# Kernel tuning notes

Hardware: AMD Instinct MI355X
Metric: run time of the kernel (lower is better)

Reference implementation:

```python
import jax, jax.numpy as jnp
import numpy as np
from jax import lax

RHO = 0.1          # init kwarg rho
CG_ITERS = 15      # dc_torch(..., 0.001, 15): fixed 15 CG iterations
EPS = 1e-12


def _c(x):  # (..., 2) real pair -> complex
    return lax.complex(x[..., 0], x[..., 1])


def _r(x):  # complex -> (..., 2) real pair
    return jnp.stack([jnp.real(x), jnp.imag(x)], axis=-1)


def fft2c(x):
    ax = (-2, -1)
    return jnp.fft.fftshift(jnp.fft.fft2(jnp.fft.ifftshift(x, axes=ax), axes=ax, norm='ortho'), axes=ax)


def ifft2c(x):
    ax = (-2, -1)
    return jnp.fft.fftshift(jnp.fft.ifft2(jnp.fft.ifftshift(x, axes=ax), axes=ax, norm='ortho'), axes=ax)


def setup_inputs() -> dict:
    key = jax.random.key(0)
    k0, k1, k2, k3 = jax.random.split(key, 4)
    B, S, C, H, W = 1, 4, 16, 320, 320
    K = jax.random.normal(k0, (B, S, C, H, W, 2), jnp.float32)
    I = jax.random.normal(k1, (B, S, H, W, 2), jnp.float32)
    csm = jax.random.normal(k2, (B, C, H, W, 2), jnp.float32) * 0.2
    mask = (jax.random.uniform(k3, (B, S, H, W)) < 0.35).astype(jnp.float32)
    return {'K_mulShot_sigCoil': K, 'I': I, 'csm': csm, 'mask': mask}


def _dc_cg(kdata, img, s, m):
    # kdata: [B,S,C,H,W] complex, img: [B,S,H,W], s: [B,C,H,W], m: [B,S,H,W]
    def E(x):                      # image [B,S,H,W] -> k-space [B,S,C,H,W]
        return m[:, :, None] * fft2c(s[:, None] * x[:, :, None])

    def EH(y):                     # adjoint: coil-combine
        return jnp.sum(jnp.conj(s)[:, None] * ifft2c(m[:, :, None] * y), axis=2)

    def AtA(x):
        return EH(E(x)) + RHO * x

    rhs = EH(kdata) + RHO * img
    x0 = jnp.zeros_like(rhs)
    r0 = rhs
    rs0 = jnp.real(jnp.vdot(r0, r0))

    def body(carry, _):
        x, r, p, rs = carry
        Ap = AtA(p)
        alpha = rs / (jnp.real(jnp.vdot(p, Ap)) + EPS)
        x = x + alpha * p
        r = r - alpha * Ap
        rs_new = jnp.real(jnp.vdot(r, r))
        p = r + (rs_new / (rs + EPS)) * p
        return (x, r, p, rs_new), None

    (x, _, _, _), _ = lax.scan(body, (x0, r0, r0, rs0), None, length=CG_ITERS)
    return x


def reference(K_mulShot_sigCoil, I, csm, mask):
    kdata = _c(K_mulShot_sigCoil)
    img = _c(I)
    s = _c(csm)
    x = _dc_cg(kdata, img, s, mask)   # image-domain CG solution
    K = fft2c(x)                      # sf.dc_torch returns k-space
    out = ifft2c(K)                   # layer returns I = ifft2c(K)
    return _r(out)
```

## Files before the change

### kernel.cpp

```cpp
#include <hip/hip_runtime.h>
#include <math.h>


#define NDIM 320
#define HHALF 160
#define HW (NDIM*NDIM)
#define NS 4
#define NC 16
#define RHO_ 0.1f
#define CG_ITERS 15

typedef float v2f __attribute__((ext_vector_type(2)));
typedef _Float16 h2 __attribute__((ext_vector_type(2)));
typedef _Float16 h8v __attribute__((ext_vector_type(8)));

__device__ __forceinline__ v2f h2f(h2 h){ return (v2f){(float)h.x, (float)h.y}; }
__device__ __forceinline__ h2 f2h(v2f v){ return (h2){(_Float16)v.x, (_Float16)v.y}; }

__device__ __forceinline__ void wsync(){
    __builtin_amdgcn_fence(__ATOMIC_ACQ_REL, "wavefront");
    __builtin_amdgcn_wave_barrier();
}

__device__ __forceinline__ float wred(float v){
    #pragma unroll
    for (int o=32;o>0;o>>=1) v += __shfl_down(v,o,64);
    return v;
}

__device__ __forceinline__ v2f cmulf(v2f a, v2f b){
    return (v2f){a.x,a.x}*b + (v2f){-a.y,a.y}*(v2f){b.y,b.x};
}

template<int SIGMA>
__device__ __forceinline__ v2f cmulw(v2f a, v2f w){
    v2f wb = (SIGMA<0) ? w : (v2f){w.x, -w.y};
    return cmulf(a, wb);
}

template<int SIGMA>
__device__ __forceinline__ v2f mulj(v2f z){
    return (v2f){ -(float)SIGMA*z.y, (float)SIGMA*z.x };
}

template<int SIGMA>
__device__ __forceinline__ void radix5(const v2f* u, v2f* v){
    const float C1 = 0.30901699437494742f, S1 = 0.95105651629515357f;
    const float C2 = -0.80901699437494745f, S2 = 0.58778525229247312f;
    v2f t1=u[1]+u[4], t2=u[2]+u[3], t3=u[1]-u[4], t4=u[2]-u[3];
    v[0] = u[0] + t1 + t2;
    v2f m1 = u[0] + t1*C1 + t2*C2;
    v2f m2 = u[0] + t1*C2 + t2*C1;
    v2f n1 = t3*S1 + t4*S2;
    v2f n2 = t3*S2 - t4*S1;
    v2f j1 = mulj<SIGMA>(n1), j2 = mulj<SIGMA>(n2);
    v[1]=m1+j1; v[4]=m1-j1; v[2]=m2+j2; v[3]=m2-j2;
}

template<int SIGMA>
__device__ __forceinline__ void dft8(const v2f* u, v2f* y){
    const float C = 0.70710678118654752f;
    v2f a0=u[0]+u[4], a1=u[0]-u[4];
    v2f a2=u[2]+u[6], a3=u[2]-u[6];
    v2f a4=u[1]+u[5], a5=u[1]-u[5];
    v2f a6=u[3]+u[7], a7=u[3]-u[7];
    v2f j3 = mulj<SIGMA>(a3);
    v2f E0=a0+a2, E2=a0-a2;
    v2f E1=a1+j3, E3=a1-j3;
    v2f j7 = mulj<SIGMA>(a7);
    v2f O0=a4+a6, O2=a4-a6;
    v2f O1=a5+j7, O3=a5-j7;
    v2f W1 = (O1 + mulj<SIGMA>(O1)) * C;
    v2f jO2 = mulj<SIGMA>(O2);
    v2f W3 = (mulj<SIGMA>(O3) - O3) * C;
    y[0]=E0+O0; y[4]=E0-O0;
    y[1]=E1+W1; y[5]=E1-W1;
    y[2]=E2+jO2; y[6]=E2-jO2;
    y[3]=E3+W3; y[7]=E3-W3;
}

template<int SIGMA>
__device__ __forceinline__ void s1_from_regs(v2f* __restrict__ A, int t,
                                             const v2f* u5){
    v2f v[5];
    radix5<SIGMA>(u5, v);
    #pragma unroll
    for (int c=0;c<5;++c) A[5*t + c] = v[c];
}

template<int SIGMA>
__device__ __forceinline__ void s1_stage(v2f* __restrict__ A, int t){
    v2f u[5];
    #pragma unroll
    for (int q=0;q<5;++q) u[q] = A[t + 64*q];
    wsync();
    s1_from_regs<SIGMA>(A, t, u);
}

template<int SIGMA>
__device__ __forceinline__ void s2_stage(v2f* __restrict__ A, int t, v2f w40){
    if (t < 40){
        v2f u[8];
        #pragma unroll
        for (int q=0;q<8;++q) u[q] = A[t + 40*q];
        wsync();
        v2f wc = w40;
        u[1] = cmulw<SIGMA>(u[1], wc);
        #pragma unroll
        for (int q=2;q<8;++q){ wc = cmulf(wc, w40); u[q] = cmulw<SIGMA>(u[q], wc); }
        v2f v[8];
        dft8<SIGMA>(u, v);
        int k = t % 5, jb = t / 5;
        int base = jb*40 + k;
        #pragma unroll
        for (int c=0;c<8;++c) A[base + 5*c] = v[c];
    }
}

template<int SIGMA>
__device__ __forceinline__ void s3_toregs(const v2f* __restrict__ A, int t,
                                          v2f w320, v2f* v){
    if (t < 40){
        v2f u[8];
        #pragma unroll
        for (int q=0;q<8;++q) u[q] = A[t + 40*q];
        v2f wc = w320;
        u[1] = cmulw<SIGMA>(u[1], wc);
        #pragma unroll
        for (int q=2;q<8;++q){ wc = cmulf(wc, w320); u[q] = cmulw<SIGMA>(u[q], wc); }
        dft8<SIGMA>(u, v);
    }
}

template<int SIGMA>
__device__ __forceinline__ void a3_fromregs(v2f* __restrict__ A, int t,
                                            v2f w320, const v2f* vin){
    if (t < 40){
        v2f u[8];
        dft8<SIGMA>(vin, u);
        v2f wc = w320;
        u[1] = cmulw<SIGMA>(u[1], wc);
        #pragma unroll
        for (int q=2;q<8;++q){ wc = cmulf(wc, w320); u[q] = cmulw<SIGMA>(u[q], wc); }
        #pragma unroll
        for (int q=0;q<8;++q) A[t + 40*q] = u[q];
    }
}

template<int SIGMA>
__device__ __forceinline__ void a2_stage(v2f* __restrict__ A, int t, v2f w40){
    if (t < 40){
        int k = t % 5, jb = t / 5;
        int base = jb*40 + k;
        v2f v[8];
        #pragma unroll
        for (int c=0;c<8;++c) v[c] = A[base + 5*c];
        wsync();
        v2f u[8];
        dft8<SIGMA>(v, u);
        v2f wc = w40;
        u[1] = cmulw<SIGMA>(u[1], wc);
        #pragma unroll
        for (int q=2;q<8;++q){ wc = cmulf(wc, w40); u[q] = cmulw<SIGMA>(u[q], wc); }
        #pragma unroll
        for (int q=0;q<8;++q) A[t + 40*q] = u[q];
    }
}

template<int SIGMA>
__device__ __forceinline__ void a1_toregs(const v2f* __restrict__ A, int t,
                                          v2f* out5){
    v2f v[5];
    #pragma unroll
    for (int c=0;c<5;++c) v[c] = A[5*t + c];
    radix5<SIGMA>(v, out5);
}

__device__ __forceinline__ void make_w(int t, v2f& w40, v2f& w320){
    float sn, cs;
    const float n2pi = -6.283185307179586f;
    __sincosf(n2pi*(float)(t%5)/40.f, &sn, &cs); w40  = (v2f){cs, sn};
    __sincosf(n2pi*(float)t/320.f,    &sn, &cs); w320 = (v2f){cs, sn};
}

__device__ __forceinline__ int sh160(int i){ return i < HHALF ? i + HHALF : i - HHALF; }

__global__ void k_prep(const v2f* __restrict__ kin, const float* __restrict__ mask,
                       const v2f* __restrict__ csm, h2* __restrict__ sP,
                       float* __restrict__ mscT, h2* __restrict__ K,
                       float* __restrict__ scal)
{
    int gid = blockIdx.x*blockDim.x + threadIdx.x;
    int gsz = gridDim.x*blockDim.x;
    if (gid < 64) scal[gid] = 0.f;
    for (int i = gid; i < NC*HW; i += gsz){
        int w = i % NDIM; int h = (i/NDIM) % NDIM; int c = i/HW;
        sP[i] = f2h(csm[(c*NDIM + sh160(h))*NDIM + sh160(w)]);
    }
    for (int i = gid; i < NS*HW; i += gsz){
        int h = i % NDIM; int wc = (i/NDIM)%NDIM; int s = i/HW;
        float m = mask[(s*NDIM + sh160(h))*NDIM + sh160(wc)];
        mscT[i] = m*m*(1.0f/102400.0f);
    }
    for (int i = gid; i < NS*NC*HW; i += gsz){
        int w = i % NDIM; int h = (i/NDIM)%NDIM; int sc = i/HW;
        int s = sc >> 4;
        int hs = sh160(h), ws = sh160(w);
        float m = mask[(s*NDIM + hs)*NDIM + ws];
        v2f kv = kin[((long)sc*NDIM + hs)*NDIM + ws];
        float f = m*(1.0f/320.0f);
        K[i] = f2h(kv * f);
    }
}

__global__ __launch_bounds__(256) void k_passA(
    const v2f* __restrict__ rv_, const v2f* __restrict__ pOld,
    v2f* __restrict__ pNew, const h2* __restrict__ sP,
    h2* __restrict__ K, float* __restrict__ scal, int iter)
{
    int bid = blockIdx.x;
    int cg = bid & 3;
    int hg = (bid>>2) % 80;
    int s  = bid / (4*80);
    int tid = threadIdx.x; int rl = tid>>6; int t = tid&63;
    int h = hg*4 + rl;
    __shared__ v2f bufA[4][NDIM];
    v2f* A = &bufA[rl][0];
    v2f w40, w320; make_w(t, w40, w320);
    float beta = 0.f;
    if (iter > 0) beta = scal[iter] / (scal[iter-1] + 1e-12f);
    long base = (long)s*HW + h*NDIM;
    v2f pv[5];
    #pragma unroll
    for (int j=0;j<5;++j){
        int idx = t + 64*j;
        v2f rr = rv_[base+idx];
        if (iter > 0){
            v2f pp = pOld[base+idx];
            pv[j] = rr + pp*beta;
        } else pv[j] = rr;
    }
    if (cg == 0){
        float d = 0.f;
        #pragma unroll
        for (int j=0;j<5;++j){
            pNew[base + t + 64*j] = pv[j];
            d += pv[j].x*pv[j].x + pv[j].y*pv[j].y;
        }
        float wd = wred(d);
        if (t==0) atomicAdd(&scal[16+iter], RHO_*wd);
    }
    int c = cg*4;
    const h2* srow = sP + (long)c*HW + h*NDIM;
    v2f sv[5];
    #pragma unroll
    for (int j=0;j<5;++j) sv[j] = h2f(srow[t+64*j]);
    #pragma unroll
    for (int c0=0;c0<4;++c0){
        v2f u5[5];
        #pragma unroll
        for (int j=0;j<5;++j) u5[j] = cmulf(sv[j], pv[j]);
        v2f sv2[5];
        if (c0<3){
            const h2* sr2 = srow + (long)(c0+1)*HW;
            #pragma unroll
            for (int j=0;j<5;++j) sv2[j] = h2f(sr2[t+64*j]);
        }
        wsync();
        s1_from_regs<-1>(A, t, u5);
        wsync();
        s2_stage<-1>(A, t, w40);
        wsync();
        v2f v8[8];
        s3_toregs<-1>(A, t, w320, v8);
        long kb = ((long)(s*NC + c + c0))*HW + h*NDIM;
        if (t < 40){
            #pragma unroll
            for (int cc=0;cc<8;++cc) K[kb + t + 40*cc] = f2h(v8[cc]);
        }
        if (c0<3){
            #pragma unroll
            for (int j=0;j<5;++j) sv[j]=sv2[j];
        }
    }
}

__global__ __launch_bounds__(1024) void k_passB(h2* __restrict__ K,
    const float* __restrict__ mscT, int doMask)
{
    constexpr int L = 324;
    int bid = blockIdx.x;
    int wt = bid % 20;
    int sc = bid / 20;
    int s = sc >> 4;
    int tid = threadIdx.x;
    int col = tid >> 6;
    int t = tid & 63;
    int w0 = wt*16;
    __shared__ v2f bufA[16][L];
    v2f w40, w320; make_w(t, w40, w320);
    float mv[8];
    if (doMask && t < 40){
        const float* mcol = mscT + (long)s*HW + (long)(w0+col)*NDIM;
        #pragma unroll
        for (int cc=0;cc<8;++cc) mv[cc] = mcol[t+40*cc];
    }
    long gb = (long)sc*HW + w0;
    for (int i = tid; i < NDIM*4; i += 1024){
        int row = i >> 2, ch = i & 3;
        h8v val = *(const h8v*)&K[gb + (long)row*NDIM + ch*4];
        #pragma unroll
        for (int k=0;k<4;++k)
            bufA[ch*4+k][row] = (v2f){(float)val[2*k], (float)val[2*k+1]};
    }
    __syncthreads();
    v2f* A = &bufA[col][0];
    if (doMask){
        s1_stage<-1>(A, t);
        wsync();
        s2_stage<-1>(A, t, w40);
        wsync();
        v2f v8[8];
        s3_toregs<-1>(A, t, w320, v8);
        if (t < 40){
            #pragma unroll
            for (int cc=0;cc<8;++cc) v8[cc] = v8[cc]*mv[cc];
        }
        wsync();
        a3_fromregs<1>(A, t, w320, v8);
        wsync();
        a2_stage<1>(A, t, w40);
        wsync();
        v2f x5[5];
        a1_toregs<1>(A, t, x5);
        wsync();
        #pragma unroll
        for (int q=0;q<5;++q) A[t + 64*q] = x5[q];
    } else {
        s1_stage<1>(A, t);
        wsync();
        s2_stage<1>(A, t, w40);
        wsync();
        v2f v8[8];
        s3_toregs<1>(A, t, w320, v8);
        wsync();
        if (t < 40){
            #pragma unroll
            for (int cc=0;cc<8;++cc) A[t + 40*cc] = v8[cc];
        }
    }
    __syncthreads();
    for (int i = tid; i < NDIM*4; i += 1024){
        int row = i >> 2, ch = i & 3;
        h8v val;
        #pragma unroll
        for (int k=0;k<4;++k){
            v2f u = bufA[ch*4+k][row];
            val[2*k] = (_Float16)u.x; val[2*k+1] = (_Float16)u.y;
        }
        *(h8v*)&K[gb + (long)row*NDIM + ch*4] = val;
    }
}

__global__ __launch_bounds__(256) void k_passC2(
    const h2* __restrict__ K, const h2* __restrict__ sP,
    const v2f* __restrict__ pVec, v2f* __restrict__ part,
    float* __restrict__ scal, int dotSlot, int doDot)
{
    int bid = blockIdx.x;
    int cg = bid & 3;
    int hg = (bid>>2) % 80;
    int s  = bid / (4*80);
    int tid = threadIdx.x; int rl = tid>>6; int t = tid&63;
    int h = hg*4 + rl;
    __shared__ v2f bufA[4][NDIM];
    __shared__ float redS[4];
    v2f* A = &bufA[rl][0];
    v2f w40, w320; make_w(t, w40, w320);
    int c = cg*4;
    long kb0 = ((long)(s*NC + c))*HW + h*NDIM;
    const h2* srow = sP + (long)c*HW + h*NDIM;
    v2f kv[8], sv[5];
    if (t < 40){
        #pragma unroll
        for (int cc=0;cc<8;++cc) kv[cc] = h2f(K[kb0 + t + 40*cc]);
    }
    #pragma unroll
    for (int j=0;j<5;++j) sv[j] = h2f(srow[t+64*j]);
    v2f acc[5];
    #pragma unroll
    for (int j=0;j<5;++j) acc[j]=(v2f){0.f,0.f};
    #pragma unroll
    for (int c0=0;c0<4;++c0){
        a3_fromregs<1>(A, t, w320, kv);
        v2f kv2[8], sv2[5];
        if (c0<3){
            long kb = kb0 + (long)(c0+1)*HW;
            const h2* sr2 = srow + (long)(c0+1)*HW;
            if (t < 40){
                #pragma unroll
                for (int cc=0;cc<8;++cc) kv2[cc] = h2f(K[kb + t + 40*cc]);
            }
            #pragma unroll
            for (int j=0;j<5;++j) sv2[j] = h2f(sr2[t+64*j]);
        }
        wsync();
        a2_stage<1>(A, t, w40);
        wsync();
        v2f x5[5];
        a1_toregs<1>(A, t, x5);
        #pragma unroll
        for (int j=0;j<5;++j){
            acc[j] += (v2f){sv[j].x,sv[j].x}*x5[j]
                    + (v2f){sv[j].y,-sv[j].y}*(v2f){x5[j].y,x5[j].x};
        }
        wsync();
        if (c0<3){
            #pragma unroll
            for (int cc=0;cc<8;++cc) kv[cc]=kv2[cc];
            #pragma unroll
            for (int j=0;j<5;++j) sv[j]=sv2[j];
        }
    }
    long pbase = (long)s*HW + h*NDIM;
    long obase = ((long)cg*NS + s)*HW + h*NDIM;
    float dot = 0.f;
    #pragma unroll
    for (int j=0;j<5;++j){
        int idx=t+64*j;
        part[obase+idx] = acc[j];
        if (doDot){
            v2f pp = pVec[pbase+idx];
            dot += pp.x*acc[j].x + pp.y*acc[j].y;
        }
    }
    if (doDot){
        float wd = wred(dot);
        if (t==0) redS[rl] = wd;
        __syncthreads();
        if (tid==0) atomicAdd(&scal[dotSlot], redS[0]+redS[1]+redS[2]+redS[3]);
    }
}

__global__ __launch_bounds__(256) void k_rhs_fin(
    const v2f* __restrict__ part, const v2f* __restrict__ Iin,
    v2f* __restrict__ r, v2f* __restrict__ x, float* __restrict__ scal)
{
    __shared__ float red[256];
    int gid = blockIdx.x*blockDim.x + threadIdx.x;
    int gsz = gridDim.x*blockDim.x;
    float rs = 0.f;
    const int NV = NS*HW;
    for (int i = gid; i < NV; i += gsz){
        int w = i % NDIM; int h = (i/NDIM)%NDIM; int s = i/HW;
        v2f iv = Iin[((long)s*NDIM + sh160(h))*NDIM + sh160(w)];
        v2f rr = part[i] + part[NV+i] + part[2*NV+i] + part[3*NV+i] + iv*RHO_;
        r[i] = rr;
        x[i] = (v2f){0.f,0.f};
        rs += rr.x*rr.x + rr.y*rr.y;
    }
    red[threadIdx.x]=rs; __syncthreads();
    for (int o=128;o>0;o>>=1){ if (threadIdx.x<o) red[threadIdx.x]+=red[threadIdx.x+o]; __syncthreads(); }
    if (threadIdx.x==0) atomicAdd(&scal[0], red[0]);
}

__global__ __launch_bounds__(256) void k_update(
    v2f* __restrict__ x, v2f* __restrict__ r,
    const v2f* __restrict__ p, const v2f* __restrict__ part,
    float* __restrict__ scal, int iter)
{
    __shared__ float red[256];
    float alpha = scal[iter] / (scal[16+iter] + 1e-12f);
    int gid = blockIdx.x*blockDim.x + threadIdx.x;
    int gsz = gridDim.x*blockDim.x;
    float rs = 0.f;
    const int NV = NS*HW;
    for (int i = gid; i < NV; i += gsz){
        v2f pvv=p[i];
        v2f av = part[i] + part[NV+i] + part[2*NV+i] + part[3*NV+i] + pvv*RHO_;
        v2f xv = x[i] + pvv*alpha;
        v2f rv = r[i] - av*alpha;
        x[i]=xv; r[i]=rv;
        rs += rv.x*rv.x + rv.y*rv.y;
    }
    red[threadIdx.x]=rs; __syncthreads();
    for (int o=128;o>0;o>>=1){ if (threadIdx.x<o) red[threadIdx.x]+=red[threadIdx.x+o]; __syncthreads(); }
    if (threadIdx.x==0) atomicAdd(&scal[iter+1], red[0]);
}

__global__ void k_final(const v2f* __restrict__ x, v2f* __restrict__ out)
{
    int gid = blockIdx.x*blockDim.x + threadIdx.x;
    int gsz = gridDim.x*blockDim.x;
    for (int i = gid; i < NS*HW; i += gsz){
        int w = i % NDIM; int h = (i/NDIM)%NDIM; int s = i/HW;
        out[i] = x[(long)s*HW + sh160(h)*NDIM + sh160(w)];
    }
}

extern "C" void kernel_launch(void* const* d_in, const int* in_sizes, int n_in,
                              void* d_out, int out_size, void* d_ws, size_t ws_size,
                              hipStream_t stream) {
    (void)in_sizes; (void)n_in; (void)out_size; (void)ws_size;
    const v2f* kin  = (const v2f*)d_in[0];
    const v2f* Iin  = (const v2f*)d_in[1];
    const v2f* csm  = (const v2f*)d_in[2];
    const float* mask = (const float*)d_in[3];

    char* w = (char*)d_ws;
    size_t off = 0;
    float* scal = (float*)(w+off);  off += 1024;
    h2* sP    = (h2*)(w+off);  off += (size_t)NC*HW*4;
    float* mscT = (float*)(w+off); off += (size_t)NS*HW*4;
    h2* K     = (h2*)(w+off);  off += (size_t)NS*NC*HW*4;
    v2f* x    = (v2f*)(w+off); off += (size_t)NS*HW*8;
    v2f* r    = (v2f*)(w+off); off += (size_t)NS*HW*8;
    v2f* pA   = (v2f*)(w+off); off += (size_t)NS*HW*8;
    v2f* pB   = (v2f*)(w+off); off += (size_t)NS*HW*8;
    v2f* part = (v2f*)(w+off); off += (size_t)4*NS*HW*8;

    k_prep<<<2048,256,0,stream>>>(kin, mask, csm, sP, mscT, K, scal);
    k_passB<<<NS*NC*20,1024,0,stream>>>(K, mscT, 0);
    k_passC2<<<NS*80*4,256,0,stream>>>(K, sP, r, part, scal, 63, 0);
    k_rhs_fin<<<640,256,0,stream>>>(part, Iin, r, x, scal);

    for (int it=0; it<CG_ITERS; ++it){
        v2f* pNew = (it&1)? pB : pA;
        v2f* pOld = (it&1)? pA : pB;
        k_passA<<<NS*80*4,256,0,stream>>>(r, pOld, pNew, sP, K, scal, it);
        k_passB<<<NS*NC*20,1024,0,stream>>>(K, mscT, 1);
        k_passC2<<<NS*80*4,256,0,stream>>>(K, sP, pNew, part, scal, 16+it, 1);
        k_update<<<640,256,0,stream>>>(x, r, pNew, part, scal, it);
    }
    k_final<<<512,256,0,stream>>>(x, (v2f*)d_out);
}
```

Measured before the change: 1.538 ms.

## Pad FFT LDS rows against bank conflicts and process two columns per wave

All shared-memory FFT buffers now use a padded row stride and a skewed index (one extra slot every 16 elements) to cut LDS bank conflicts in the strided radix-5/radix-8 stage accesses. In the column-FFT kernel each wavefront now handles two columns, with reads and writes of the two columns interleaved, and the block shrinks from 1024 to 512 threads with a higher occupancy hint. This is meant to raise instruction-level parallelism and LDS throughput. The cost is more registers per thread, plus one extra wave barrier per stage from splitting each stage into separate read and write phases.

```diff
diff --git a/kernel.cpp b/kernel.cpp
--- a/kernel.cpp
+++ b/kernel.cpp
@@ -9,6 +9,7 @@
 #define NC 16
 #define RHO_ 0.1f
 #define CG_ITERS 15
+#define LPAD 341
 
 typedef float v2f __attribute__((ext_vector_type(2)));
 typedef _Float16 h2 __attribute__((ext_vector_type(2)));
@@ -16,6 +17,8 @@
 
 __device__ __forceinline__ v2f h2f(h2 h){ return (v2f){(float)h.x, (float)h.y}; }
 __device__ __forceinline__ h2 f2h(v2f v){ return (h2){(_Float16)v.x, (_Float16)v.y}; }
+
+__device__ __forceinline__ int ix(int i){ return i + (i>>4); }
 
 __device__ __forceinline__ void wsync(){
     __builtin_amdgcn_fence(__ATOMIC_ACQ_REL, "wavefront");
@@ -79,31 +82,26 @@
     y[3]=E3+W3; y[7]=E3-W3;
 }
 
-template<int SIGMA>
-__device__ __forceinline__ void s1_from_regs(v2f* __restrict__ A, int t,
-                                             const v2f* u5){
+__device__ __forceinline__ void s1_read(const v2f* __restrict__ A, int t, v2f* u){
+    #pragma unroll
+    for (int q=0;q<5;++q) u[q] = A[ix(t + 64*q)];
+}
+template<int SIGMA>
+__device__ __forceinline__ void s1_write(v2f* __restrict__ A, int t, const v2f* u5){
     v2f v[5];
     radix5<SIGMA>(u5, v);
     #pragma unroll
-    for (int c=0;c<5;++c) A[5*t + c] = v[c];
-}
-
-template<int SIGMA>
-__device__ __forceinline__ void s1_stage(v2f* __restrict__ A, int t){
-    v2f u[5];
-    #pragma unroll
-    for (int q=0;q<5;++q) u[q] = A[t + 64*q];
-    wsync();
-    s1_from_regs<SIGMA>(A, t, u);
-}
-
-template<int SIGMA>
-__device__ __forceinline__ void s2_stage(v2f* __restrict__ A, int t, v2f w40){
-    if (t < 40){
-        v2f u[8];
-        #pragma unroll
-        for (int q=0;q<8;++q) u[q] = A[t + 40*q];
-        wsync();
+    for (int c=0;c<5;++c) A[ix(5*t + c)] = v[c];
+}
+__device__ __forceinline__ void s2_read(const v2f* __restrict__ A, int t, v2f* u){
+    if (t < 40){
+        #pragma unroll
+        for (int q=0;q<8;++q) u[q] = A[ix(t + 40*q)];
+    }
+}
+template<int SIGMA>
+__device__ __forceinline__ void s2_write(v2f* __restrict__ A, int t, v2f w40, v2f* u){
+    if (t < 40){
         v2f wc = w40;
         u[1] = cmulw<SIGMA>(u[1], wc);
         #pragma unroll
@@ -113,17 +111,16 @@
         int k = t % 5, jb = t / 5;
         int base = jb*40 + k;
         #pragma unroll
-        for (int c=0;c<8;++c) A[base + 5*c] = v[c];
-    }
-}
-
+        for (int c=0;c<8;++c) A[ix(base + 5*c)] = v[c];
+    }
+}
 template<int SIGMA>
 __device__ __forceinline__ void s3_toregs(const v2f* __restrict__ A, int t,
                                           v2f w320, v2f* v){
     if (t < 40){
         v2f u[8];
         #pragma unroll
-        for (int q=0;q<8;++q) u[q] = A[t + 40*q];
+        for (int q=0;q<8;++q) u[q] = A[ix(t + 40*q)];
         v2f wc = w320;
         u[1] = cmulw<SIGMA>(u[1], wc);
         #pragma unroll
@@ -131,7 +128,6 @@
         dft8<SIGMA>(u, v);
     }
 }
-
 template<int SIGMA>
 __device__ __forceinline__ void a3_fromregs(v2f* __restrict__ A, int t,
                                             v2f w320, const v2f* vin){
@@ -143,19 +139,20 @@
         #pragma unroll
         for (int q=2;q<8;++q){ wc = cmulf(wc, w320); u[q] = cmulw<SIGMA>(u[q], wc); }
         #pragma unroll
-        for (int q=0;q<8;++q) A[t + 40*q] = u[q];
-    }
-}
-
-template<int SIGMA>
-__device__ __forceinline__ void a2_stage(v2f* __restrict__ A, int t, v2f w40){
+        for (int q=0;q<8;++q) A[ix(t + 40*q)] = u[q];
+    }
+}
+__device__ __forceinline__ void a2_read(const v2f* __restrict__ A, int t, v2f* v){
     if (t < 40){
         int k = t % 5, jb = t / 5;
         int base = jb*40 + k;
-        v2f v[8];
-        #pragma unroll
-        for (int c=0;c<8;++c) v[c] = A[base + 5*c];
-        wsync();
+        #pragma unroll
+        for (int c=0;c<8;++c) v[c] = A[ix(base + 5*c)];
+    }
+}
+template<int SIGMA>
+__device__ __forceinline__ void a2_write(v2f* __restrict__ A, int t, v2f w40, v2f* v){
+    if (t < 40){
         v2f u[8];
         dft8<SIGMA>(v, u);
         v2f wc = w40;
@@ -163,16 +160,15 @@
         #pragma unroll
         for (int q=2;q<8;++q){ wc = cmulf(wc, w40); u[q] = cmulw<SIGMA>(u[q], wc); }
         #pragma unroll
-        for (int q=0;q<8;++q) A[t + 40*q] = u[q];
-    }
-}
-
+        for (int q=0;q<8;++q) A[ix(t + 40*q)] = u[q];
+    }
+}
 template<int SIGMA>
 __device__ __forceinline__ void a1_toregs(const v2f* __restrict__ A, int t,
                                           v2f* out5){
     v2f v[5];
     #pragma unroll
-    for (int c=0;c<5;++c) v[c] = A[5*t + c];
+    for (int c=0;c<5;++c) v[c] = A[ix(5*t + c)];
     radix5<SIGMA>(v, out5);
 }
 
@@ -224,7 +220,7 @@
     int s  = bid / (4*80);
     int tid = threadIdx.x; int rl = tid>>6; int t = tid&63;
     int h = hg*4 + rl;
-    __shared__ v2f bufA[4][NDIM];
+    __shared__ v2f bufA[4][LPAD];
     v2f* A = &bufA[rl][0];
     v2f w40, w320; make_w(t, w40, w320);
     float beta = 0.f;
@@ -267,9 +263,12 @@
             for (int j=0;j<5;++j) sv2[j] = h2f(sr2[t+64*j]);
         }
         wsync();
-        s1_from_regs<-1>(A, t, u5);
-        wsync();
-        s2_stage<-1>(A, t, w40);
+        s1_write<-1>(A, t, u5);
+        wsync();
+        v2f u8[8];
+        s2_read(A, t, u8);
+        wsync();
+        s2_write<-1>(A, t, w40, u8);
         wsync();
         v2f v8[8];
         s3_toregs<-1>(A, t, w320, v8);
@@ -285,77 +284,93 @@
     }
 }
 
-__global__ __launch_bounds__(1024) void k_passB(h2* __restrict__ K,
+__global__ __launch_bounds__(512,4) void k_passB(h2* __restrict__ K,
     const float* __restrict__ mscT, int doMask)
 {
-    constexpr int L = 324;
     int bid = blockIdx.x;
     int wt = bid % 20;
     int sc = bid / 20;
     int s = sc >> 4;
     int tid = threadIdx.x;
-    int col = tid >> 6;
+    int wv = tid >> 6;
     int t = tid & 63;
     int w0 = wt*16;
-    __shared__ v2f bufA[16][L];
+    __shared__ v2f bufA[16][LPAD];
     v2f w40, w320; make_w(t, w40, w320);
-    float mv[8];
+    float mvA[8], mvB[8];
     if (doMask && t < 40){
-        const float* mcol = mscT + (long)s*HW + (long)(w0+col)*NDIM;
-        #pragma unroll
-        for (int cc=0;cc<8;++cc) mv[cc] = mcol[t+40*cc];
+        const float* mA = mscT + (long)s*HW + (long)(w0+2*wv)*NDIM;
+        const float* mB = mA + NDIM;
+        #pragma unroll
+        for (int cc=0;cc<8;++cc){ mvA[cc] = mA[t+40*cc]; mvB[cc] = mB[t+40*cc]; }
     }
     long gb = (long)sc*HW + w0;
-    for (int i = tid; i < NDIM*4; i += 1024){
+    for (int i = tid; i < NDIM*4; i += 512){
         int row = i >> 2, ch = i & 3;
         h8v val = *(const h8v*)&K[gb + (long)row*NDIM + ch*4];
         #pragma unroll
         for (int k=0;k<4;++k)
-            bufA[ch*4+k][row] = (v2f){(float)val[2*k], (float)val[2*k+1]};
+            bufA[ch*4+k][ix(row)] = (v2f){(float)val[2*k], (float)val[2*k+1]};
     }
     __syncthreads();
-    v2f* A = &bufA[col][0];
+    v2f* A0 = &bufA[2*wv][0];
+    v2f* A1 = &bufA[2*wv+1][0];
     if (doMask){
-        s1_stage<-1>(A, t);
-        wsync();
-        s2_stage<-1>(A, t, w40);
-        wsync();
-        v2f v8[8];
-        s3_toregs<-1>(A, t, w320, v8);
+        v2f uA[5], uB[5];
+        s1_read(A0, t, uA); s1_read(A1, t, uB);
+        wsync();
+        s1_write<-1>(A0, t, uA); s1_write<-1>(A1, t, uB);
+        wsync();
+        v2f u8A[8], u8B[8];
+        s2_read(A0, t, u8A); s2_read(A1, t, u8B);
+        wsync();
+        s2_write<-1>(A0, t, w40, u8A); s2_write<-1>(A1, t, w40, u8B);
+        wsync();
+        v2f v8A[8], v8B[8];
+        s3_toregs<-1>(A0, t, w320, v8A); s3_toregs<-1>(A1, t, w320, v8B);
         if (t < 40){
             #pragma unroll
-            for (int cc=0;cc<8;++cc) v8[cc] = v8[cc]*mv[cc];
-        }
-        wsync();
-        a3_fromregs<1>(A, t, w320, v8);
-        wsync();
-        a2_stage<1>(A, t, w40);
-        wsync();
-        v2f x5[5];
-        a1_toregs<1>(A, t, x5);
-        wsync();
-        #pragma unroll
-        for (int q=0;q<5;++q) A[t + 64*q] = x5[q];
+            for (int cc=0;cc<8;++cc){ v8A[cc] = v8A[cc]*mvA[cc]; v8B[cc] = v8B[cc]*mvB[cc]; }
+        }
+        wsync();
+        a3_fromregs<1>(A0, t, w320, v8A); a3_fromregs<1>(A1, t, w320, v8B);
+        wsync();
+        v2f r8A[8], r8B[8];
+        a2_read(A0, t, r8A); a2_read(A1, t, r8B);
+        wsync();
+        a2_write<1>(A0, t, w40, r8A); a2_write<1>(A1, t, w40, r8B);
+        wsync();
+        v2f x5A[5], x5B[5];
+        a1_toregs<1>(A0, t, x5A); a1_toregs<1>(A1, t, x5B);
+        wsync();
+        #pragma unroll
+        for (int q=0;q<5;++q){ A0[ix(t + 64*q)] = x5A[q]; A1[ix(t + 64*q)] = x5B[q]; }
     } else {
-        s1_stage<1>(A, t);
-        wsync();
-        s2_stage<1>(A, t, w40);
-        wsync();
-        v2f v8[8];
-        s3_toregs<1>(A, t, w320, v8);
+        v2f uA[5], uB[5];
+        s1_read(A0, t, uA); s1_read(A1, t, uB);
+        wsync();
+        s1_write<1>(A0, t, uA); s1_write<1>(A1, t, uB);
+        wsync();
+        v2f u8A[8], u8B[8];
+        s2_read(A0, t, u8A); s2_read(A1, t, u8B);
+        wsync();
+        s2_write<1>(A0, t, w40, u8A); s2_write<1>(A1, t, w40, u8B);
+        wsync();
+        v2f v8A[8], v8B[8];
+        s3_toregs<1>(A0, t, w320, v8A); s3_toregs<1>(A1, t, w320, v8B);
         wsync();
         if (t < 40){
             #pragma unroll
-            for (int cc=0;cc<8;++cc) A[t + 40*cc] = v8[cc];
+            for (int cc=0;cc<8;++cc){ A0[ix(t + 40*cc)] = v8A[cc]; A1[ix(t + 40*cc)] = v8B[cc]; }
         }
     }
     __syncthreads();
-    for (int i = tid; i < NDIM*4; i += 1024){
+    for (int i = tid; i < NDIM*4; i += 512){
         int row = i >> 2, ch = i & 3;
         h8v val;
         #pragma unroll
         for (int k=0;k<4;++k){
-            v2f u = bufA[ch*4+k][row];
+            v2f u = bufA[ch*4+k][ix(row)];
             val[2*k] = (_Float16)u.x; val[2*k+1] = (_Float16)u.y;
         }
         *(h8v*)&K[gb + (long)row*NDIM + ch*4] = val;
@@ -373,7 +388,7 @@
     int s  = bid / (4*80);
     int tid = threadIdx.x; int rl = tid>>6; int t = tid&63;
     int h = hg*4 + rl;
-    __shared__ v2f bufA[4][NDIM];
+    __shared__ v2f bufA[4][LPAD];
     __shared__ float redS[4];
     v2f* A = &bufA[rl][0];
     v2f w40, w320; make_w(t, w40, w320);
@@ -405,7 +420,10 @@
             for (int j=0;j<5;++j) sv2[j] = h2f(sr2[t+64*j]);
         }
         wsync();
-        a2_stage<1>(A, t, w40);
+        v2f r8[8];
+        a2_read(A, t, r8);
+        wsync();
+        a2_write<1>(A, t, w40, r8);
         wsync();
         v2f x5[5];
         a1_toregs<1>(A, t, x5);
@@ -520,7 +538,7 @@
     v2f* part = (v2f*)(w+off); off += (size_t)4*NS*HW*8;
 
     k_prep<<<2048,256,0,stream>>>(kin, mask, csm, sP, mscT, K, scal);
-    k_passB<<<NS*NC*20,1024,0,stream>>>(K, mscT, 0);
+    k_passB<<<NS*NC*20,512,0,stream>>>(K, mscT, 0);
     k_passC2<<<NS*80*4,256,0,stream>>>(K, sP, r, part, scal, 63, 0);
     k_rhs_fin<<<640,256,0,stream>>>(part, Iin, r, x, scal);
 
@@ -528,7 +546,7 @@
         v2f* pNew = (it&1)? pB : pA;
         v2f* pOld = (it&1)? pA : pB;
         k_passA<<<NS*80*4,256,0,stream>>>(r, pOld, pNew, sP, K, scal, it);
-        k_passB<<<NS*NC*20,1024,0,stream>>>(K, mscT, 1);
+        k_passB<<<NS*NC*20,512,0,stream>>>(K, mscT, 1);
         k_passC2<<<NS*80*4,256,0,stream>>>(K, sP, pNew, part, scal, 16+it, 1);
         k_update<<<640,256,0,stream>>>(x, r, pNew, part, scal, it);
     }
```

Result: slower. 1.683 ms (+9.4%).
